# Performance work log

Measured on AMD Instinct MI355X. Metric: run time of the kernel, lower is better.

The kernel has to match this reference:

```python
import jax, jax.numpy as jnp
import numpy as np

B, T, IN, H, Z, DH, K = 512, 256, 5, 256, 128, 512, 20
OUT = 6 * K + 3


def setup_inputs() -> dict:
    key = jax.random.key(0)
    ks = jax.random.split(key, 24)
    p = lambda k, shp: jax.random.normal(k, shp, dtype=jnp.float32) * 0.05
    return {
        "s": jax.random.normal(ks[0], (B, T, IN), dtype=jnp.float32),
        "epsilon": jax.random.normal(ks[1], (Z,), dtype=jnp.float32),
        "Wih_f": p(ks[2], (4 * H, IN)), "Whh_f": p(ks[3], (4 * H, H)),
        "bih_f": p(ks[4], (4 * H,)), "bhh_f": p(ks[5], (4 * H,)),
        "Wih_b": p(ks[6], (4 * H, IN)), "Whh_b": p(ks[7], (4 * H, H)),
        "bih_b": p(ks[8], (4 * H,)), "bhh_b": p(ks[9], (4 * H,)),
        "W_sigma": p(ks[10], (Z, 2 * H)), "b_sigma": p(ks[11], (Z,)),
        "W_mu": p(ks[12], (Z, 2 * H)), "b_mu": p(ks[13], (Z,)),
        "W_h0": p(ks[14], (DH, Z)), "b_h0": p(ks[15], (DH,)),
        "Wih_d": p(ks[16], (4 * DH, IN + Z)), "Whh_d": p(ks[17], (4 * DH, DH)),
        "bih_d": p(ks[18], (4 * DH,)), "bhh_d": p(ks[19], (4 * DH,)),
        "W_dec": p(ks[20], (OUT, DH)), "b_dec": p(ks[21], (OUT,)),
    }


def _lstm_scan(x, Wih, Whh, b, reverse):
    # x: [T, B, in]; PyTorch gate order i, f, g, o
    Hh = Whh.shape[1]
    h0 = jnp.zeros((x.shape[1], Hh), x.dtype)

    def step(carry, xt):
        h, c = carry
        g = xt @ Wih.T + h @ Whh.T + b
        i, f, gg, o = jnp.split(g, 4, axis=-1)
        c = jax.nn.sigmoid(f) * c + jax.nn.sigmoid(i) * jnp.tanh(gg)
        h = jax.nn.sigmoid(o) * jnp.tanh(c)
        return (h, c), h

    _, hs = jax.lax.scan(step, (h0, h0), x, reverse=reverse)
    return hs  # [T, B, Hh]


def _mdn(y):
    # y: [..., 123] -> per-mixture (pi, mu1, mu2, sx, sy, corr) + 3 pen logits
    mix = y[..., :6 * K].reshape(y.shape[:-1] + (K, 6))
    pi = jax.nn.softmax(mix[..., 0], axis=-1)
    out_mix = jnp.stack(
        [pi, mix[..., 1], mix[..., 2], jnp.exp(mix[..., 3]),
         jnp.exp(mix[..., 4]), jnp.tanh(mix[..., 5])], axis=-1)
    pen = jax.nn.softmax(y[..., 6 * K:], axis=-1)
    return jnp.concatenate([out_mix.reshape(y.shape[:-1] + (6 * K,)), pen], axis=-1)


def reference(s, epsilon, Wih_f, Whh_f, bih_f, bhh_f, Wih_b, Whh_b, bih_b, bhh_b,
              W_sigma, b_sigma, W_mu, b_mu, W_h0, b_h0,
              Wih_d, Whh_d, bih_d, bhh_d, W_dec, b_dec):
    x = jnp.transpose(s, (1, 0, 2))  # [T, B, 5]
    hf = _lstm_scan(x, Wih_f, Whh_f, bih_f + bhh_f, False)
    hb = _lstm_scan(x, Wih_b, Whh_b, bih_b + bhh_b, True)
    h = jnp.concatenate([hf[-1], hb[-1]], axis=-1)  # output at last time step, [B, 512]
    presig = h @ W_sigma.T + b_sigma
    mu = h @ W_mu.T + b_mu
    sigma = jnp.exp(presig / 2)
    z = mu + sigma * epsilon  # [B, Z]
    h0 = jnp.tanh(z @ W_h0.T + b_h0)
    c0 = jnp.zeros((s.shape[0], DH), s.dtype)
    s0 = jnp.tile(jnp.array([0.0, 0.0, 1.0, 0.0, 0.0], s.dtype), (s.shape[0], 1))
    dec_in = jnp.concatenate([s0[None], x[:T - 1]], axis=0)  # [T, B, 5]
    bdec = bih_d + bhh_d

    def step(carry, st):
        hh, cc = carry
        xt = jnp.concatenate([st, z], axis=-1)  # [B, 133]
        g = xt @ Wih_d.T + hh @ Whh_d.T + bdec
        i, f, gg, o = jnp.split(g, 4, axis=-1)
        cc = jax.nn.sigmoid(f) * cc + jax.nn.sigmoid(i) * jnp.tanh(gg)
        hh = jax.nn.sigmoid(o) * jnp.tanh(cc)
        y = hh @ W_dec.T + b_dec
        return (hh, cc), y

    _, ys = jax.lax.scan(step, (h0, c0), dec_in)  # [T, B, 123]
    output = _mdn(jnp.transpose(ys, (1, 0, 2)))   # [B, T, 123]
    return (output, mu, presig)
```

## Files before the change

kernel.cpp:

```cpp
#include <hip/hip_runtime.h>

typedef unsigned short u16;
typedef unsigned long long u64;
typedef __attribute__((ext_vector_type(8))) short bfrag;
typedef __attribute__((ext_vector_type(4))) float f32x4;

#define MFMA __builtin_amdgcn_mfma_f32_16x16x32_bf16

#define OFF_FLAGS 0ull
#define OFF_HENC  4096ull
#define OFF_WENC  528384ull
#define OFF_WDEC  1118208ull
#define OFF_WY    3870720ull
#define OFF_WMS   4001792ull
#define OFF_WH0   4280320ull
#define OFF_HDEC  4444160ull
#define OFF_HLAT  5492736ull
#define OFF_AZ    6049792ull
#define OFF_SX    6213632ull

__device__ __forceinline__ u16 f2bf(float f) {
  union { float f; unsigned int i; } v; v.f = f;
  unsigned int r = v.i + 0x7fffu + ((v.i >> 16) & 1u);
  return (u16)(r >> 16);
}
__device__ __forceinline__ float sigm(float x) { return 1.0f / (1.0f + __expf(-x)); }
__device__ __forceinline__ float tanh_(float x) {
  float a = fabsf(x);
  float e = __expf(-2.0f * a);
  float r = (1.0f - e) / (1.0f + e);
  return x < 0.0f ? -r : r;
}

__device__ __forceinline__ u64 aload(const u64* p) {
  return __hip_atomic_load(p, __ATOMIC_RELAXED, __HIP_MEMORY_SCOPE_AGENT);
}
__device__ __forceinline__ void astore(u64* p, u64 v) {
  __hip_atomic_store(p, v, __ATOMIC_RELAXED, __HIP_MEMORY_SCOPE_AGENT);
}
__device__ __forceinline__ float afload(const float* p) {
  return __hip_atomic_load(p, __ATOMIC_RELAXED, __HIP_MEMORY_SCOPE_AGENT);
}
__device__ __forceinline__ void afstore(float* p, float v) {
  __hip_atomic_store(p, v, __ATOMIC_RELAXED, __HIP_MEMORY_SCOPE_AGENT);
}

__device__ __forceinline__ void gwait(int* base, int ep, int tid, int* sdead) {
  if (ep > 0) {
    if (tid < 32 && *sdead == 0) {
      int* fp = base + tid;
      int spin = 0;
      while (__hip_atomic_load(fp, __ATOMIC_RELAXED, __HIP_MEMORY_SCOPE_AGENT) < ep) {
        __builtin_amdgcn_s_sleep(1);
        if (++spin > (1 << 18)) { *sdead = 1; break; }
      }
    }
  }
  __syncthreads();
  asm volatile("" ::: "memory");
}
__device__ __forceinline__ void garrive(int* base, int m, int ep, int tid) {
  asm volatile("s_waitcnt vmcnt(0)" ::: "memory");
  __syncthreads();
  if (tid == 0)
    __hip_atomic_store(base + m, ep, __ATOMIC_RELAXED, __HIP_MEMORY_SCOPE_AGENT);
}

__global__ void pack_wenc(const float* __restrict__ Whh, const float* __restrict__ Wih,
                          const float* __restrict__ bi, const float* __restrict__ bh,
                          u16* __restrict__ out) {
  int idx = blockIdx.x * 256 + threadIdx.x;
  if (idx >= 294912) return;
  int m = idx / 9216, within = idx % 9216;
  int kb = within >> 10, rest = within & 1023;
  int ng = rest >> 9, l = (rest >> 3) & 63, j = rest & 7;
  int nl = ng * 16 + (l & 15);
  int u = nl >> 2, g = nl & 3;
  int row = g * 256 + m * 8 + u;
  int k = kb * 32 + (l >> 4) * 8 + j;
  float v = 0.f;
  if (k < 256) v = Whh[row * 256 + k];
  else if (k < 261) v = Wih[row * 5 + (k - 256)];
  else if (k == 261) v = bi[row] + bh[row];
  out[idx] = f2bf(v);
}

__global__ void pack_wdec(const float* __restrict__ Whh, const float* __restrict__ Wih,
                          const float* __restrict__ bi, const float* __restrict__ bh,
                          u16* __restrict__ out) {
  int idx = blockIdx.x * 256 + threadIdx.x;
  if (idx >= 1376256) return;
  int m = idx / 43008, within = idx % 43008;
  int kb = within >> 11, rest = within & 2047;
  int w = rest >> 9, l = (rest >> 3) & 63, j = rest & 7;
  int nl = w * 16 + (l & 15);
  int u = nl >> 2, g = nl & 3;
  int row = g * 512 + m * 16 + u;
  int k = kb * 32 + (l >> 4) * 8 + j;
  float v = 0.f;
  if (k < 512) v = Whh[row * 512 + k];
  else if (k < 640) v = Wih[row * 133 + 5 + (k - 512)];
  else if (k < 645) v = Wih[row * 133 + (k - 640)];
  else if (k == 645) v = bi[row] + bh[row];
  out[idx] = f2bf(v);
}

__global__ void pack_wy(const float* __restrict__ Wd, u16* __restrict__ out) {
  int idx = blockIdx.x * 256 + threadIdx.x;
  if (idx >= 65536) return;
  int m = idx >> 13, within = idx & 8191;
  int kb = within >> 9, rest = within & 511;
  int l = rest >> 3, j = rest & 7;
  int row = m * 16 + (l & 15);
  int k = kb * 32 + (l >> 4) * 8 + j;
  float v = (row < 123 && k < 512) ? Wd[row * 512 + k] : 0.f;
  out[idx] = f2bf(v);
}

__global__ void pack_wms(const float* __restrict__ Wmu, const float* __restrict__ bmu,
                         const float* __restrict__ Wsig, const float* __restrict__ bsig,
                         u16* __restrict__ out) {
  int idx = blockIdx.x * 256 + threadIdx.x;
  if (idx >= 139264) return;
  int r = idx / 544, k = idx % 544;
  float v = 0.f;
  if (r < 128) {
    if (k < 512) v = Wmu[r * 512 + k];
    else if (k == 512) v = bmu[r];
  } else {
    int r2 = r - 128;
    if (k < 512) v = Wsig[r2 * 512 + k];
    else if (k == 512) v = bsig[r2];
  }
  out[idx] = f2bf(v);
}

__global__ void pack_wh0(const float* __restrict__ Wh0, const float* __restrict__ bh0,
                         u16* __restrict__ out) {
  int idx = blockIdx.x * 256 + threadIdx.x;
  if (idx >= 81920) return;
  int r = idx / 160, k = idx % 160;
  float v = 0.f;
  if (k < 128) v = Wh0[r * 128 + k];
  else if (k == 128) v = bh0[r];
  out[idx] = f2bf(v);
}

__global__ void pack_sx(const float* __restrict__ s, u16* __restrict__ out) {
  int idx = blockIdx.x * 256 + threadIdx.x;
  if (idx >= 1048576) return;
  int j = idx & 7, b = (idx >> 3) & 511, t = idx >> 12;
  u16 v;
  if (j < 5) v = f2bf(s[((size_t)b * 256 + t) * 5 + j]);
  else v = (j == 5) ? (u16)0x3F80 : (u16)0;
  out[idx] = v;
}

__global__ __launch_bounds__(256, 1) void rnn_persist(
    int* __restrict__ flags, u16* __restrict__ henc,
    const u16* __restrict__ WENCP, const u16* __restrict__ WDECP,
    const u16* __restrict__ WYP, const u16* __restrict__ WMSP, const u16* __restrict__ WH0P,
    u16* __restrict__ hdec, u16* __restrict__ hlat, u16* __restrict__ Az,
    const u16* __restrict__ SXD,
    const float* __restrict__ s, const float* __restrict__ eps,
    const float* __restrict__ Wih_b, const float* __restrict__ bih_b,
    const float* __restrict__ bhh_b,
    const float* __restrict__ b_dec, float* __restrict__ out)
{
  __shared__ __align__(16) u16 sm[72960];
  __shared__ __align__(16) float gbuf[2112];
  __shared__ __align__(16) u16 hst[1024];
  __shared__ int sdead;

  const int tid = threadIdx.x;
  const int blk = blockIdx.x;
  const int g = blk & 7;
  const int m = blk >> 3;
  const int B0 = g * 64;
  const int w = tid >> 6, l = tid & 63;
  const int lr = l & 15, ko = (l >> 4) * 8;
  int* FA = flags + g * 128;
  int* FB = FA + 64;

  float* out_mu = out + 16121856;
  float* out_ps = out + 16187392;

  const int gcol = m * 16 + lr;
  float bd = 0.f;
  if (m < 8 && gcol < 123) bd = b_dec[gcol];

  if (tid == 0) sdead = 0;
  {
    bfrag zz = {0, 0, 0, 0, 0, 0, 0, 0};
    #pragma unroll
    for (int i = 0; i < 5; ++i) {
      int c = i * 256 + tid;
      if (c < 1184) *(bfrag*)(sm + c * 8) = zz;
    }
  }
  {
    const u16* src = WENCP + (size_t)m * 9216;
    #pragma unroll
    for (int i = 0; i < 5; ++i) {
      int c = i * 256 + tid;
      if (c < 1152) *(bfrag*)(sm + 21760 + c * 8) = *(const bfrag*)(src + c * 8);
    }
  }
  __syncthreads();

  float c_enc0 = 0.f, c_enc1 = 0.f;
  #pragma unroll 1
  for (int t = 0; t < 256; ++t) {
    #pragma unroll
    for (int X = 0; X < 2; ++X) {
      int* F = X ? FB : FA;
      gwait(F, t, tid, &sdead);
      const u64* hs = (const u64*)(henc + (size_t)((t + 1) & 1) * 131072 +
                                   (size_t)(B0 + X * 32) * 256);
      u64 hv[8];
      #pragma unroll
      for (int i = 0; i < 8; ++i) hv[i] = aload(hs + i * 256 + tid);
      #pragma unroll
      for (int i = 0; i < 8; ++i) {
        int idx = i * 256 + tid;
        *(u64*)(sm + (idx >> 6) * 296 + (idx & 63) * 4) = hv[i];
      }
      if (tid < 64) {
        int row = tid >> 1, q = tid & 1;
        *(u64*)(sm + row * 296 + 256 + q * 4) =
            *(const u64*)(SXD + ((size_t)(t * 512 + B0 + X * 32 + row)) * 8 + q * 4);
      }
      __syncthreads();
      const int mt = w >> 1, ng = w & 1;
      f32x4 acc = {0.f, 0.f, 0.f, 0.f};
      #pragma unroll
      for (int kb = 0; kb < 9; ++kb) {
        bfrag a = *(const bfrag*)(sm + (mt * 16 + lr) * 296 + kb * 32 + ko);
        bfrag bw = *(const bfrag*)(sm + 21760 + (kb * 2 + ng) * 512 + l * 8);
        acc = MFMA(a, bw, acc, 0, 0, 0);
      }
      #pragma unroll
      for (int j = 0; j < 4; ++j)
        gbuf[(mt * 16 + (l >> 4) * 4 + j) * 33 + ng * 16 + lr] = acc[j];
      __syncthreads();
      {
        int bl = tid >> 3, u = tid & 7;
        float gi = gbuf[bl * 33 + u * 4 + 0], gf = gbuf[bl * 33 + u * 4 + 1];
        float gg = gbuf[bl * 33 + u * 4 + 2], go = gbuf[bl * 33 + u * 4 + 3];
        float cprev = (X == 0) ? c_enc0 : c_enc1;
        float c = sigm(gf) * cprev + sigm(gi) * tanh_(gg);
        if (X == 0) c_enc0 = c; else c_enc1 = c;
        hst[bl * 8 + u] = f2bf(sigm(go) * tanh_(c));
      }
      __syncthreads();
      if (tid < 64) {
        int row = tid >> 1, q = tid & 1;
        u64 v = *(const u64*)(hst + row * 8 + q * 4);
        astore((u64*)(henc + (size_t)(t & 1) * 131072 +
                      (size_t)(B0 + X * 32 + row) * 256 + m * 8) + q, v);
      }
      garrive(F, m, t + 1, tid);
    }
  }

  u16* lat_hf = (u16*)gbuf;
  u16* lat_hb = (u16*)gbuf + 512;
  u16* lat_z  = (u16*)gbuf + 1024;

  gwait(FA, 256, tid, &sdead);
  gwait(FB, 256, tid, &sdead);
  {
    const u16* src = WDECP + (size_t)m * 43008;
    #pragma unroll 1
    for (int i = 0; i < 21; ++i) {
      int c = i * 256 + tid;
      *(bfrag*)(sm + 21760 + c * 8) = *(const bfrag*)(src + c * 8);
    }
  }
  if (m < 8) {
    const u16* src = WYP + (size_t)m * 8192;
    #pragma unroll
    for (int i = 0; i < 4; ++i) {
      int c = i * 256 + tid;
      *(bfrag*)(sm + 64768 + c * 8) = *(const bfrag*)(src + c * 8);
    }
  }
  #pragma unroll
  for (int r = 0; r < 2; ++r) {
    int b = B0 + m * 2 + r;
    if (tid < 64) {
      u64 v = aload((const u64*)(henc + 131072 + (size_t)b * 256) + tid);
      *(u64*)(lat_hf + r * 256 + tid * 4) = v;
    }
    {
      const float* xr = s + ((size_t)b * 256 + 255) * 5;
      float x0 = xr[0], x1 = xr[1], x2 = xr[2], x3 = xr[3], x4 = xr[4];
      int n = tid;
      float gv[4];
      #pragma unroll
      for (int gg = 0; gg < 4; ++gg) {
        int row = gg * 256 + n;
        gv[gg] = bih_b[row] + bhh_b[row] + x0 * Wih_b[row * 5] + x1 * Wih_b[row * 5 + 1] +
                 x2 * Wih_b[row * 5 + 2] + x3 * Wih_b[row * 5 + 3] + x4 * Wih_b[row * 5 + 4];
      }
      float c = sigm(gv[0]) * tanh_(gv[2]);
      lat_hb[r * 256 + n] = f2bf(sigm(gv[3]) * tanh_(c));
    }
  }
  __syncthreads();
  #pragma unroll
  for (int it = 0; it < 2; ++it) {
    int idx = it * 256 + tid;
    if (idx < 272) {
      int rr = idx / 136, u = idx % 136;
      u64 pv = 0;
      #pragma unroll
      for (int q = 0; q < 4; ++q) {
        int c = u * 4 + q;
        u16 x;
        if (c < 256) x = lat_hf[rr * 256 + c];
        else if (c < 512) x = lat_hb[rr * 256 + c - 256];
        else if (c == 512) x = 0x3F80;
        else x = 0;
        pv |= ((u64)x) << (q * 16);
      }
      astore((u64*)(hlat + (size_t)(B0 + m * 2 + rr) * 544) + u, pv);
    }
  }
  garrive(FA, m, 257, tid);

  gwait(FA, 257, tid, &sdead);
  {
    const int bH = m >> 4, cT = m & 15;
    const u64* src = (const u64*)(hlat + (size_t)(B0 + bH * 32) * 544);
    u64 sv[17];
    #pragma unroll
    for (int i = 0; i < 17; ++i) sv[i] = aload(src + i * 256 + tid);
    #pragma unroll
    for (int i = 0; i < 17; ++i) *(u64*)(sm + (i * 256 + tid) * 4) = sv[i];
    __syncthreads();
    if (w < 2) {
      f32x4 acc = {0.f, 0.f, 0.f, 0.f};
      const u16* bp = WMSP + (size_t)(cT * 16 + lr) * 544 + ko;
      #pragma unroll
      for (int kb = 0; kb < 17; ++kb) {
        bfrag a = *(const bfrag*)(sm + (w * 16 + lr) * 544 + kb * 32 + ko);
        bfrag bb = *(const bfrag*)(bp + kb * 32);
        acc = MFMA(a, bb, acc, 0, 0, 0);
      }
      int nc = cT * 16 + lr;
      #pragma unroll
      for (int j = 0; j < 4; ++j) {
        int b = B0 + bH * 32 + w * 16 + (l >> 4) * 4 + j;
        if (nc < 128) afstore(out_mu + (size_t)b * 128 + nc, acc[j]);
        else afstore(out_ps + (size_t)b * 128 + nc - 128, acc[j]);
      }
    }
  }
  garrive(FA, m, 258, tid);

  gwait(FA, 258, tid, &sdead);
  {
    int r = tid >> 7, zj = tid & 127;
    int b = B0 + m * 2 + r;
    float mu = afload(out_mu + (size_t)b * 128 + zj);
    float ps = afload(out_ps + (size_t)b * 128 + zj);
    float z = mu + __expf(0.5f * ps) * eps[zj];
    lat_z[r * 128 + zj] = f2bf(z);
  }
  __syncthreads();
  if (tid < 80) {
    int r = tid / 40, u = tid % 40;
    u64 pv = 0;
    #pragma unroll
    for (int q = 0; q < 4; ++q) {
      int c = u * 4 + q;
      u16 x;
      if (c < 128) x = lat_z[r * 128 + c];
      else if (c == 128) x = 0x3F80;
      else x = 0;
      pv |= ((u64)x) << (q * 16);
    }
    astore((u64*)(Az + (size_t)(B0 + m * 2 + r) * 160) + u, pv);
  }
  garrive(FA, m, 259, tid);

  gwait(FA, 259, tid, &sdead);
  u64 zreg0[4], zreg1[4];
  {
    int r = tid >> 3;
    #pragma unroll
    for (int i = 0; i < 4; ++i) {
      int uu = (tid & 7) * 4 + i;
      zreg0[i] = aload((const u64*)(Az + (size_t)(B0 + r) * 160) + uu);
      zreg1[i] = aload((const u64*)(Az + (size_t)(B0 + 32 + r) * 160) + uu);
    }
  }
  {
    const u64* src = (const u64*)(Az + (size_t)B0 * 160);
    u64 sv[10];
    #pragma unroll
    for (int i = 0; i < 10; ++i) sv[i] = aload(src + i * 256 + tid);
    #pragma unroll
    for (int i = 0; i < 10; ++i) *(u64*)(sm + (i * 256 + tid) * 4) = sv[i];
    __syncthreads();
    f32x4 acc = {0.f, 0.f, 0.f, 0.f};
    const u16* bp = WH0P + (size_t)(m * 16 + lr) * 160 + ko;
    #pragma unroll
    for (int kb = 0; kb < 5; ++kb) {
      bfrag a = *(const bfrag*)(sm + (w * 16 + lr) * 160 + kb * 32 + ko);
      bfrag bb = *(const bfrag*)(bp + kb * 32);
      acc = MFMA(a, bb, acc, 0, 0, 0);
    }
    #pragma unroll
    for (int j = 0; j < 4; ++j)
      hst[(w * 16 + (l >> 4) * 4 + j) * 16 + lr] = f2bf(tanh_(acc[j]));
  }
  __syncthreads();
  #pragma unroll
  for (int i = 0; i < 5; ++i) {
    int idx = i * 256 + tid;
    if (idx < 1120) {
      int row = idx / 35, c = idx % 35;
      sm[row * 680 + 645 + c] = (c == 0) ? 0x3F80 : 0;
    }
  }
  {
    int row = tid >> 2, q = tid & 3;
    u64 v = *(const u64*)(hst + row * 16 + q * 4);
    astore((u64*)(hdec + 262144 + (size_t)(B0 + row) * 512 + m * 16) + q, v);
  }
  garrive(FA, m, 260, tid);
  if (tid == 0)
    __hip_atomic_store(FB + m, 257, __ATOMIC_RELAXED, __HIP_MEMORY_SCOPE_AGENT);

  float c_dec00 = 0.f, c_dec01 = 0.f, c_dec10 = 0.f, c_dec11 = 0.f;
  #pragma unroll 1
  for (int t = 0; t < 256; ++t) {
    #pragma unroll
    for (int X = 0; X < 2; ++X) {
      int* F = X ? FB : FA;
      int base = X ? 257 : 260;
      gwait(F, base + t, tid, &sdead);
      const u64* hs = (const u64*)(hdec + (size_t)((t + 1) & 1) * 262144 +
                                   (size_t)(B0 + X * 32) * 512);
      u64 hv[16];
      #pragma unroll
      for (int i = 0; i < 16; ++i) hv[i] = aload(hs + i * 256 + tid);
      #pragma unroll
      for (int i = 0; i < 16; ++i) {
        int idx = i * 256 + tid;
        *(u64*)(sm + (idx >> 7) * 680 + (idx & 127) * 4) = hv[i];
      }
      {
        int r = tid >> 3;
        #pragma unroll
        for (int i = 0; i < 4; ++i) {
          int uu = (tid & 7) * 4 + i;
          *(u64*)(sm + r * 680 + 512 + uu * 4) = (X == 0) ? zreg0[i] : zreg1[i];
        }
      }
      if (tid < 64) {
        int row = tid >> 1, q = tid & 1;
        u64 v;
        if (t == 0) v = q ? 0x000000003F800000ULL : 0x00003F8000000000ULL;
        else v = *(const u64*)(SXD + ((size_t)((t - 1) * 512 + B0 + X * 32 + row)) * 8 + q * 4);
        *(u64*)(sm + row * 680 + 640 + q * 4) = v;
      }
      __syncthreads();
      const int mtd = w & 1, nb = (w >> 1) * 2;
      const bool doy = (m < 8) && (w < 2) && (t > 0);
      f32x4 acc0 = {0.f, 0.f, 0.f, 0.f}, acc1 = {0.f, 0.f, 0.f, 0.f}, accy = {0.f, 0.f, 0.f, 0.f};
      #pragma unroll
      for (int kb = 0; kb < 21; ++kb) {
        bfrag a  = *(const bfrag*)(sm + (mtd * 16 + lr) * 680 + kb * 32 + ko);
        bfrag b0 = *(const bfrag*)(sm + 21760 + kb * 2048 + nb * 512 + l * 8);
        bfrag b1 = *(const bfrag*)(sm + 21760 + kb * 2048 + (nb + 1) * 512 + l * 8);
        acc0 = MFMA(a, b0, acc0, 0, 0, 0);
        acc1 = MFMA(a, b1, acc1, 0, 0, 0);
        if (kb < 16 && doy) {
          bfrag by = *(const bfrag*)(sm + 64768 + kb * 512 + l * 8);
          accy = MFMA(a, by, accy, 0, 0, 0);
        }
      }
      if (doy && gcol < 123) {
        int brow = B0 + X * 32 + w * 16 + (l >> 4) * 4;
        #pragma unroll
        for (int j = 0; j < 4; ++j)
          out[((size_t)(brow + j) * 256 + (t - 1)) * 123 + gcol] = accy[j] + bd;
      }
      #pragma unroll
      for (int j = 0; j < 4; ++j) {
        int grow = mtd * 16 + (l >> 4) * 4 + j;
        gbuf[grow * 66 + nb * 16 + lr] = acc0[j];
        gbuf[grow * 66 + (nb + 1) * 16 + lr] = acc1[j];
      }
      __syncthreads();
      #pragma unroll
      for (int p = 0; p < 2; ++p) {
        int idx = p * 256 + tid;
        int bl = idx >> 4, u = idx & 15;
        float gi = gbuf[bl * 66 + u * 4 + 0], gf = gbuf[bl * 66 + u * 4 + 1];
        float gg = gbuf[bl * 66 + u * 4 + 2], go = gbuf[bl * 66 + u * 4 + 3];
        float cprev = (X == 0) ? (p == 0 ? c_dec00 : c_dec01) : (p == 0 ? c_dec10 : c_dec11);
        float c = sigm(gf) * cprev + sigm(gi) * tanh_(gg);
        if (X == 0) { if (p == 0) c_dec00 = c; else c_dec01 = c; }
        else        { if (p == 0) c_dec10 = c; else c_dec11 = c; }
        hst[bl * 16 + u] = f2bf(sigm(go) * tanh_(c));
      }
      __syncthreads();
      if (tid < 128) {
        int row = tid >> 2, q = tid & 3;
        u64 v = *(const u64*)(hst + row * 16 + q * 4);
        astore((u64*)(hdec + (size_t)(t & 1) * 262144 +
                      (size_t)(B0 + X * 32 + row) * 512 + m * 16) + q, v);
      }
      garrive(F, m, base + t + 1, tid);
    }
  }

  gwait(FA, 516, tid, &sdead);
  gwait(FB, 513, tid, &sdead);
  #pragma unroll
  for (int X = 0; X < 2; ++X) {
    const u64* hsrc = (const u64*)(hdec + 262144 + (size_t)(B0 + X * 32) * 512);
    u64 hv[16];
    #pragma unroll
    for (int i = 0; i < 16; ++i) hv[i] = aload(hsrc + i * 256 + tid);
    #pragma unroll
    for (int i = 0; i < 16; ++i) {
      int idx = i * 256 + tid;
      *(u64*)(sm + (idx >> 7) * 680 + (idx & 127) * 4) = hv[i];
    }
    __syncthreads();
    if (m < 8 && w < 2) {
      f32x4 accy = {0.f, 0.f, 0.f, 0.f};
      #pragma unroll
      for (int kb = 0; kb < 16; ++kb) {
        bfrag a = *(const bfrag*)(sm + (w * 16 + lr) * 680 + kb * 32 + ko);
        bfrag by = *(const bfrag*)(sm + 64768 + kb * 512 + l * 8);
        accy = MFMA(a, by, accy, 0, 0, 0);
      }
      if (gcol < 123) {
        int brow = B0 + X * 32 + w * 16 + (l >> 4) * 4;
        #pragma unroll
        for (int j = 0; j < 4; ++j)
          out[((size_t)(brow + j) * 256 + 255) * 123 + gcol] = accy[j] + bd;
      }
    }
    __syncthreads();
  }
}

__global__ __launch_bounds__(64) void mdn_final(float* __restrict__ out) {
  __shared__ float rows[64 * 123];
  const int tid = threadIdx.x;
  float4* g4 = (float4*)(out + (size_t)blockIdx.x * 64 * 123);
  #pragma unroll
  for (int i = 0; i < 31; ++i) {
    int c = i * 64 + tid;
    if (c < 1968) ((float4*)rows)[c] = g4[c];
  }
  __syncthreads();
  {
    float* r = rows + tid * 123;
    float m1 = -1e30f;
    #pragma unroll
    for (int k = 0; k < 20; ++k) m1 = fmaxf(m1, r[6 * k]);
    float s1 = 0.f;
    #pragma unroll
    for (int k = 0; k < 20; ++k) s1 += __expf(r[6 * k] - m1);
    float i1 = 1.f / s1;
    #pragma unroll
    for (int k = 0; k < 20; ++k) {
      r[6 * k] = __expf(r[6 * k] - m1) * i1;
      r[6 * k + 3] = __expf(r[6 * k + 3]);
      r[6 * k + 4] = __expf(r[6 * k + 4]);
      r[6 * k + 5] = tanh_(r[6 * k + 5]);
    }
    float p0 = r[120], p1 = r[121], p2 = r[122];
    float mp = fmaxf(p0, fmaxf(p1, p2));
    float e0 = __expf(p0 - mp), e1 = __expf(p1 - mp), e2 = __expf(p2 - mp);
    float ip = 1.f / (e0 + e1 + e2);
    r[120] = e0 * ip; r[121] = e1 * ip; r[122] = e2 * ip;
  }
  __syncthreads();
  #pragma unroll
  for (int i = 0; i < 31; ++i) {
    int c = i * 64 + tid;
    if (c < 1968) g4[c] = ((float4*)rows)[c];
  }
}

extern "C" void kernel_launch(void* const* d_in, const int* in_sizes, int n_in,
                              void* d_out, int out_size, void* d_ws, size_t ws_size,
                              hipStream_t stream) {
  const float* s       = (const float*)d_in[0];
  const float* eps     = (const float*)d_in[1];
  const float* Wih_f   = (const float*)d_in[2];
  const float* Whh_f   = (const float*)d_in[3];
  const float* bih_f   = (const float*)d_in[4];
  const float* bhh_f   = (const float*)d_in[5];
  const float* Wih_b   = (const float*)d_in[6];
  const float* bih_b   = (const float*)d_in[8];
  const float* bhh_b   = (const float*)d_in[9];
  const float* W_sigma = (const float*)d_in[10];
  const float* b_sigma = (const float*)d_in[11];
  const float* W_mu    = (const float*)d_in[12];
  const float* b_mu    = (const float*)d_in[13];
  const float* W_h0    = (const float*)d_in[14];
  const float* b_h0    = (const float*)d_in[15];
  const float* Wih_d   = (const float*)d_in[16];
  const float* Whh_d   = (const float*)d_in[17];
  const float* bih_d   = (const float*)d_in[18];
  const float* bhh_d   = (const float*)d_in[19];
  const float* W_dec   = (const float*)d_in[20];
  const float* b_dec   = (const float*)d_in[21];

  char* ws = (char*)d_ws;
  int* FLAGS  = (int*)(ws + OFF_FLAGS);
  u16* HENC   = (u16*)(ws + OFF_HENC);
  u16* WENCP  = (u16*)(ws + OFF_WENC);
  u16* WDECP  = (u16*)(ws + OFF_WDEC);
  u16* WYP    = (u16*)(ws + OFF_WY);
  u16* WMSP   = (u16*)(ws + OFF_WMS);
  u16* WH0P   = (u16*)(ws + OFF_WH0);
  u16* HDEC   = (u16*)(ws + OFF_HDEC);
  u16* HLAT   = (u16*)(ws + OFF_HLAT);
  u16* AZ     = (u16*)(ws + OFF_AZ);
  u16* SXD    = (u16*)(ws + OFF_SX);
  float* out  = (float*)d_out;

  hipMemsetAsync(ws, 0, 4096 + 524288, stream);

  pack_wenc<<<1152, 256, 0, stream>>>(Whh_f, Wih_f, bih_f, bhh_f, WENCP);
  pack_wdec<<<5376, 256, 0, stream>>>(Whh_d, Wih_d, bih_d, bhh_d, WDECP);
  pack_wy<<<256, 256, 0, stream>>>(W_dec, WYP);
  pack_wms<<<544, 256, 0, stream>>>(W_mu, b_mu, W_sigma, b_sigma, WMSP);
  pack_wh0<<<320, 256, 0, stream>>>(W_h0, b_h0, WH0P);
  pack_sx<<<4096, 256, 0, stream>>>(s, SXD);

  rnn_persist<<<256, 256, 0, stream>>>(FLAGS, HENC, WENCP, WDECP, WYP, WMSP, WH0P,
                                       HDEC, HLAT, AZ, SXD, s, eps,
                                       Wih_b, bih_b, bhh_b, b_dec, out);

  mdn_final<<<2048, 64, 0, stream>>>(out);

  (void)in_sizes; (void)n_in; (void)out_size; (void)ws_size;
}
```

Baseline: 2.991 ms.

## Replace per-step flag barriers with timestamp-tagged hidden-state words and prefetch

Each bf16 pair of hidden state is now stored as a 64-bit word whose high half carries the timestep tag. Consumers spin on the tags of the data itself instead of waiting on separate arrive/wait flag counters per step. The next step's hidden state and inputs are loaded right after the current step's store, so the load latency overlaps with other blocks finishing. This removes a flag round-trip per recurrent step. The cost is twice the bytes per hidden-state transfer, more registers (32 u64), and a larger memset of the workspace.

Result: no change. 2.943 ms, median of 2 (-1.6%).

```diff
diff --git a/kernel.cpp b/kernel.cpp
--- a/kernel.cpp
+++ b/kernel.cpp
@@ -1,6 +1,7 @@
 #include <hip/hip_runtime.h>
 
 typedef unsigned short u16;
+typedef unsigned int u32;
 typedef unsigned long long u64;
 typedef __attribute__((ext_vector_type(8))) short bfrag;
 typedef __attribute__((ext_vector_type(4))) float f32x4;
@@ -8,16 +9,17 @@
 #define MFMA __builtin_amdgcn_mfma_f32_16x16x32_bf16
 
 #define OFF_FLAGS 0ull
-#define OFF_HENC  4096ull
-#define OFF_WENC  528384ull
-#define OFF_WDEC  1118208ull
-#define OFF_WY    3870720ull
-#define OFF_WMS   4001792ull
-#define OFF_WH0   4280320ull
-#define OFF_HDEC  4444160ull
-#define OFF_HLAT  5492736ull
-#define OFF_AZ    6049792ull
-#define OFF_SX    6213632ull
+#define OFF_HENCW 4096ull
+#define OFF_HDECW 1052672ull
+#define MEMSET_BYTES 3149824ull
+#define OFF_WENC  3149824ull
+#define OFF_WDEC  3739648ull
+#define OFF_WY    6492160ull
+#define OFF_WMS   6623232ull
+#define OFF_WH0   6901760ull
+#define OFF_HLAT  7065600ull
+#define OFF_AZ    7622656ull
+#define OFF_SX    7786496ull
 
 __device__ __forceinline__ u16 f2bf(float f) {
   union { float f; unsigned int i; } v; v.f = f;
@@ -157,11 +159,10 @@
 }
 
 __global__ __launch_bounds__(256, 1) void rnn_persist(
-    int* __restrict__ flags, u16* __restrict__ henc,
+    int* __restrict__ flags, u64* __restrict__ hencW, u64* __restrict__ hdecW,
     const u16* __restrict__ WENCP, const u16* __restrict__ WDECP,
     const u16* __restrict__ WYP, const u16* __restrict__ WMSP, const u16* __restrict__ WH0P,
-    u16* __restrict__ hdec, u16* __restrict__ hlat, u16* __restrict__ Az,
-    const u16* __restrict__ SXD,
+    u16* __restrict__ hlat, u16* __restrict__ Az, const u16* __restrict__ SXD,
     const float* __restrict__ s, const float* __restrict__ eps,
     const float* __restrict__ Wih_b, const float* __restrict__ bih_b,
     const float* __restrict__ bhh_b,
@@ -179,8 +180,8 @@
   const int B0 = g * 64;
   const int w = tid >> 6, l = tid & 63;
   const int lr = l & 15, ko = (l >> 4) * 8;
-  int* FA = flags + g * 128;
-  int* FB = FA + 64;
+  int* FG = flags + g * 64;
+  const u32* hst32 = (const u32*)hst;
 
   float* out_mu = out + 16121856;
   float* out_ps = out + 16187392;
@@ -208,67 +209,83 @@
   }
   __syncthreads();
 
+  u64 hv[32];
+  u64 sxv = 0;
+
+  {
+    const u64* base = hencW + 65536 + (size_t)B0 * 128;
+    #pragma unroll
+    for (int i = 0; i < 16; ++i) hv[i] = aload(base + i * 256 + tid);
+    if (tid < 64)
+      sxv = *(const u64*)(SXD + (size_t)(B0 + (tid >> 1)) * 8 + (tid & 1) * 4);
+  }
   float c_enc0 = 0.f, c_enc1 = 0.f;
   #pragma unroll 1
-  for (int t = 0; t < 256; ++t) {
-    #pragma unroll
-    for (int X = 0; X < 2; ++X) {
-      int* F = X ? FB : FA;
-      gwait(F, t, tid, &sdead);
-      const u64* hs = (const u64*)(henc + (size_t)((t + 1) & 1) * 131072 +
-                                   (size_t)(B0 + X * 32) * 256);
-      u64 hv[8];
-      #pragma unroll
-      for (int i = 0; i < 8; ++i) hv[i] = aload(hs + i * 256 + tid);
-      #pragma unroll
-      for (int i = 0; i < 8; ++i) {
-        int idx = i * 256 + tid;
-        *(u64*)(sm + (idx >> 6) * 296 + (idx & 63) * 4) = hv[i];
-      }
-      if (tid < 64) {
-        int row = tid >> 1, q = tid & 1;
-        *(u64*)(sm + row * 296 + 256 + q * 4) =
-            *(const u64*)(SXD + ((size_t)(t * 512 + B0 + X * 32 + row)) * 8 + q * 4);
-      }
-      __syncthreads();
-      const int mt = w >> 1, ng = w & 1;
-      f32x4 acc = {0.f, 0.f, 0.f, 0.f};
-      #pragma unroll
-      for (int kb = 0; kb < 9; ++kb) {
-        bfrag a = *(const bfrag*)(sm + (mt * 16 + lr) * 296 + kb * 32 + ko);
-        bfrag bw = *(const bfrag*)(sm + 21760 + (kb * 2 + ng) * 512 + l * 8);
-        acc = MFMA(a, bw, acc, 0, 0, 0);
-      }
-      #pragma unroll
-      for (int j = 0; j < 4; ++j)
-        gbuf[(mt * 16 + (l >> 4) * 4 + j) * 33 + ng * 16 + lr] = acc[j];
-      __syncthreads();
-      {
-        int bl = tid >> 3, u = tid & 7;
-        float gi = gbuf[bl * 33 + u * 4 + 0], gf = gbuf[bl * 33 + u * 4 + 1];
-        float gg = gbuf[bl * 33 + u * 4 + 2], go = gbuf[bl * 33 + u * 4 + 3];
-        float cprev = (X == 0) ? c_enc0 : c_enc1;
-        float c = sigm(gf) * cprev + sigm(gi) * tanh_(gg);
-        if (X == 0) c_enc0 = c; else c_enc1 = c;
-        hst[bl * 8 + u] = f2bf(sigm(go) * tanh_(c));
-      }
-      __syncthreads();
-      if (tid < 64) {
-        int row = tid >> 1, q = tid & 1;
-        u64 v = *(const u64*)(hst + row * 8 + q * 4);
-        astore((u64*)(henc + (size_t)(t & 1) * 131072 +
-                      (size_t)(B0 + X * 32 + row) * 256 + m * 8) + q, v);
-      }
-      garrive(F, m, t + 1, tid);
+  for (int e = 0; e < 512; ++e) {
+    const int X = e & 1, t = e >> 1;
+    {
+      const u64* base = hencW + (size_t)((t + 1) & 1) * 65536 + (size_t)(B0 + X * 32) * 128;
+      int tries = 0;
+      while (true) {
+        bool ok = true;
+        #pragma unroll
+        for (int i = 0; i < 16; ++i) ok &= ((u32)(hv[i] >> 32) == (u32)t);
+        if (__all(ok)) break;
+        if (++tries > (1 << 14)) break;
+        __builtin_amdgcn_s_sleep(1);
+        #pragma unroll
+        for (int i = 0; i < 16; ++i) hv[i] = aload(base + i * 256 + tid);
+      }
+    }
+    #pragma unroll
+    for (int i = 0; i < 16; ++i) {
+      int idx = i * 256 + tid;
+      *(u32*)((char*)sm + (idx >> 7) * 592 + (idx & 127) * 4) = (u32)hv[i];
+    }
+    if (tid < 64) *(u64*)(sm + (tid >> 1) * 296 + 256 + (tid & 1) * 4) = sxv;
+    __syncthreads();
+    const int mt = w >> 1, ng = w & 1;
+    f32x4 acc = {0.f, 0.f, 0.f, 0.f};
+    #pragma unroll
+    for (int kb = 0; kb < 9; ++kb) {
+      bfrag a = *(const bfrag*)(sm + (mt * 16 + lr) * 296 + kb * 32 + ko);
+      bfrag bw = *(const bfrag*)(sm + 21760 + (kb * 2 + ng) * 512 + l * 8);
+      acc = MFMA(a, bw, acc, 0, 0, 0);
+    }
+    #pragma unroll
+    for (int j = 0; j < 4; ++j)
+      gbuf[(mt * 16 + (l >> 4) * 4 + j) * 33 + ng * 16 + lr] = acc[j];
+    __syncthreads();
+    {
+      int bl = tid >> 3, u = tid & 7;
+      float gi = gbuf[bl * 33 + u * 4 + 0], gf = gbuf[bl * 33 + u * 4 + 1];
+      float gg = gbuf[bl * 33 + u * 4 + 2], go = gbuf[bl * 33 + u * 4 + 3];
+      float cprev = (X == 0) ? c_enc0 : c_enc1;
+      float c = sigm(gf) * cprev + sigm(gi) * tanh_(gg);
+      if (X == 0) c_enc0 = c; else c_enc1 = c;
+      hst[bl * 8 + u] = f2bf(sigm(go) * tanh_(c));
+    }
+    __syncthreads();
+    if (tid < 128) {
+      int row = tid >> 2, j = tid & 3;
+      u64 wv = (u64)hst32[row * 4 + j] | ((u64)(u32)(t + 1) << 32);
+      astore(hencW + (size_t)(t & 1) * 65536 + (size_t)(B0 + X * 32 + row) * 128 + 4 * m + j, wv);
+    }
+    if (e < 511) {
+      int Xn = (e + 1) & 1, tn = (e + 1) >> 1;
+      const u64* base = hencW + (size_t)((tn + 1) & 1) * 65536 + (size_t)(B0 + Xn * 32) * 128;
+      #pragma unroll
+      for (int i = 0; i < 16; ++i) hv[i] = aload(base + i * 256 + tid);
+      if (tid < 64)
+        sxv = *(const u64*)(SXD + (size_t)(tn * 512 + B0 + Xn * 32 + (tid >> 1)) * 8 + (tid & 1) * 4);
     }
   }
 
   u16* lat_hf = (u16*)gbuf;
   u16* lat_hb = (u16*)gbuf + 512;
   u16* lat_z  = (u16*)gbuf + 1024;
-
-  gwait(FA, 256, tid, &sdead);
-  gwait(FB, 256, tid, &sdead);
+  __syncthreads();
+
   {
     const u16* src = WDECP + (size_t)m * 43008;
     #pragma unroll 1
@@ -285,27 +302,33 @@
       *(bfrag*)(sm + 64768 + c * 8) = *(const bfrag*)(src + c * 8);
     }
   }
+  {
+    int r = tid >> 7, wc = tid & 127;
+    const u64* p = hencW + 65536 + (size_t)(B0 + m * 2 + r) * 128 + wc;
+    u64 v = aload(p);
+    int tries = 0;
+    while (!__all((u32)(v >> 32) == 256u)) {
+      if (++tries > (1 << 14)) break;
+      __builtin_amdgcn_s_sleep(1);
+      v = aload(p);
+    }
+    ((u32*)lat_hf)[r * 128 + wc] = (u32)v;
+  }
   #pragma unroll
   for (int r = 0; r < 2; ++r) {
     int b = B0 + m * 2 + r;
-    if (tid < 64) {
-      u64 v = aload((const u64*)(henc + 131072 + (size_t)b * 256) + tid);
-      *(u64*)(lat_hf + r * 256 + tid * 4) = v;
-    }
-    {
-      const float* xr = s + ((size_t)b * 256 + 255) * 5;
-      float x0 = xr[0], x1 = xr[1], x2 = xr[2], x3 = xr[3], x4 = xr[4];
-      int n = tid;
-      float gv[4];
-      #pragma unroll
-      for (int gg = 0; gg < 4; ++gg) {
-        int row = gg * 256 + n;
-        gv[gg] = bih_b[row] + bhh_b[row] + x0 * Wih_b[row * 5] + x1 * Wih_b[row * 5 + 1] +
-                 x2 * Wih_b[row * 5 + 2] + x3 * Wih_b[row * 5 + 3] + x4 * Wih_b[row * 5 + 4];
-      }
-      float c = sigm(gv[0]) * tanh_(gv[2]);
-      lat_hb[r * 256 + n] = f2bf(sigm(gv[3]) * tanh_(c));
-    }
+    const float* xr = s + ((size_t)b * 256 + 255) * 5;
+    float x0 = xr[0], x1 = xr[1], x2 = xr[2], x3 = xr[3], x4 = xr[4];
+    int n = tid;
+    float gv[4];
+    #pragma unroll
+    for (int gg = 0; gg < 4; ++gg) {
+      int row = gg * 256 + n;
+      gv[gg] = bih_b[row] + bhh_b[row] + x0 * Wih_b[row * 5] + x1 * Wih_b[row * 5 + 1] +
+               x2 * Wih_b[row * 5 + 2] + x3 * Wih_b[row * 5 + 3] + x4 * Wih_b[row * 5 + 4];
+    }
+    float c = sigm(gv[0]) * tanh_(gv[2]);
+    lat_hb[r * 256 + n] = f2bf(sigm(gv[3]) * tanh_(c));
   }
   __syncthreads();
   #pragma unroll
@@ -327,9 +350,8 @@
       astore((u64*)(hlat + (size_t)(B0 + m * 2 + rr) * 544) + u, pv);
     }
   }
-  garrive(FA, m, 257, tid);
-
-  gwait(FA, 257, tid, &sdead);
+  garrive(FG, m, 1, tid);
+  gwait(FG, 1, tid, &sdead);
   {
     const int bH = m >> 4, cT = m & 15;
     const u64* src = (const u64*)(hlat + (size_t)(B0 + bH * 32) * 544);
@@ -357,9 +379,8 @@
       }
     }
   }
-  garrive(FA, m, 258, tid);
-
-  gwait(FA, 258, tid, &sdead);
+  garrive(FG, m, 2, tid);
+  gwait(FG, 2, tid, &sdead);
   {
     int r = tid >> 7, zj = tid & 127;
     int b = B0 + m * 2 + r;
@@ -383,9 +404,8 @@
     }
     astore((u64*)(Az + (size_t)(B0 + m * 2 + r) * 160) + u, pv);
   }
-  garrive(FA, m, 259, tid);
-
-  gwait(FA, 259, tid, &sdead);
+  garrive(FG, m, 3, tid);
+  gwait(FG, 3, tid, &sdead);
   u64 zreg0[4], zreg1[4];
   {
     int r = tid >> 3;
@@ -418,119 +438,147 @@
   }
   __syncthreads();
   #pragma unroll
-  for (int i = 0; i < 5; ++i) {
+  for (int i = 0; i < 2; ++i) {
     int idx = i * 256 + tid;
-    if (idx < 1120) {
-      int row = idx / 35, c = idx % 35;
-      sm[row * 680 + 645 + c] = (c == 0) ? 0x3F80 : 0;
-    }
-  }
-  {
-    int row = tid >> 2, q = tid & 3;
-    u64 v = *(const u64*)(hst + row * 16 + q * 4);
-    astore((u64*)(hdec + 262144 + (size_t)(B0 + row) * 512 + m * 16) + q, v);
-  }
-  garrive(FA, m, 260, tid);
-  if (tid == 0)
-    __hip_atomic_store(FB + m, 257, __ATOMIC_RELAXED, __HIP_MEMORY_SCOPE_AGENT);
-
-  float c_dec00 = 0.f, c_dec01 = 0.f, c_dec10 = 0.f, c_dec11 = 0.f;
+    int row = idx >> 3, j = idx & 7;
+    u64 wv = (u64)hst32[row * 8 + j] | (1ull << 32);
+    astore(hdecW + 131072 + (size_t)(B0 + row) * 256 + 8 * m + j, wv);
+  }
+  #pragma unroll
+  for (int i = 0; i < 4; ++i) {
+    int idx = i * 256 + tid;
+    if (idx < 1024) {
+      int row = idx >> 5, c = idx & 31;
+      sm[row * 680 + 648 + c] = 0;
+    }
+  }
+  garrive(FG, m, 4, tid);
+  gwait(FG, 4, tid, &sdead);
+
+  {
+    const u64* base = hdecW + 131072 + (size_t)B0 * 256;
+    #pragma unroll
+    for (int i = 0; i < 32; ++i) hv[i] = aload(base + i * 256 + tid);
+    if (tid < 64)
+      sxv = *(const u64*)(SXD + (size_t)(B0 + (tid >> 1)) * 8 + (tid & 1) * 4);
+  }
+  float c00 = 0.f, c01 = 0.f, c10 = 0.f, c11 = 0.f;
   #pragma unroll 1
-  for (int t = 0; t < 256; ++t) {
-    #pragma unroll
-    for (int X = 0; X < 2; ++X) {
-      int* F = X ? FB : FA;
-      int base = X ? 257 : 260;
-      gwait(F, base + t, tid, &sdead);
-      const u64* hs = (const u64*)(hdec + (size_t)((t + 1) & 1) * 262144 +
-                                   (size_t)(B0 + X * 32) * 512);
-      u64 hv[16];
-      #pragma unroll
-      for (int i = 0; i < 16; ++i) hv[i] = aload(hs + i * 256 + tid);
-      #pragma unroll
-      for (int i = 0; i < 16; ++i) {
-        int idx = i * 256 + tid;
-        *(u64*)(sm + (idx >> 7) * 680 + (idx & 127) * 4) = hv[i];
-      }
-      {
-        int r = tid >> 3;
+  for (int e = 0; e < 512; ++e) {
+    const int X = e & 1, t = e >> 1;
+    {
+      const u64* base = hdecW + (size_t)((t + 1) & 1) * 131072 + (size_t)(B0 + X * 32) * 256;
+      int tries = 0;
+      while (true) {
+        bool ok = true;
         #pragma unroll
-        for (int i = 0; i < 4; ++i) {
-          int uu = (tid & 7) * 4 + i;
-          *(u64*)(sm + r * 680 + 512 + uu * 4) = (X == 0) ? zreg0[i] : zreg1[i];
-        }
-      }
+        for (int i = 0; i < 32; ++i) ok &= ((u32)(hv[i] >> 32) == (u32)(t + 1));
+        if (__all(ok)) break;
+        if (++tries > (1 << 14)) break;
+        __builtin_amdgcn_s_sleep(1);
+        #pragma unroll
+        for (int i = 0; i < 32; ++i) hv[i] = aload(base + i * 256 + tid);
+      }
+    }
+    #pragma unroll
+    for (int i = 0; i < 32; ++i) {
+      int idx = i * 256 + tid;
+      *(u32*)((char*)sm + (idx >> 8) * 1360 + (idx & 255) * 4) = (u32)hv[i];
+    }
+    {
+      int r = tid >> 3;
+      #pragma unroll
+      for (int i = 0; i < 4; ++i) {
+        int uu = (tid & 7) * 4 + i;
+        *(u64*)(sm + r * 680 + 512 + uu * 4) = (X == 0) ? zreg0[i] : zreg1[i];
+      }
+    }
+    if (tid < 64) {
+      u64 v = sxv;
+      if (t == 0) v = (tid & 1) ? 0x000000003F800000ULL : 0x00003F8000000000ULL;
+      *(u64*)(sm + (tid >> 1) * 680 + 640 + (tid & 1) * 4) = v;
+    }
+    __syncthreads();
+    const int mtd = w & 1, nb = (w >> 1) * 2;
+    const bool doy = (m < 8) && (w < 2) && (t > 0);
+    f32x4 acc0 = {0.f, 0.f, 0.f, 0.f}, acc1 = {0.f, 0.f, 0.f, 0.f}, accy = {0.f, 0.f, 0.f, 0.f};
+    #pragma unroll
+    for (int kb = 0; kb < 21; ++kb) {
+      bfrag a  = *(const bfrag*)(sm + (mtd * 16 + lr) * 680 + kb * 32 + ko);
+      bfrag b0 = *(const bfrag*)(sm + 21760 + kb * 2048 + nb * 512 + l * 8);
+      bfrag b1 = *(const bfrag*)(sm + 21760 + kb * 2048 + (nb + 1) * 512 + l * 8);
+      acc0 = MFMA(a, b0, acc0, 0, 0, 0);
+      acc1 = MFMA(a, b1, acc1, 0, 0, 0);
+      if (kb < 16 && doy) {
+        bfrag by = *(const bfrag*)(sm + 64768 + kb * 512 + l * 8);
+        accy = MFMA(a, by, accy, 0, 0, 0);
+      }
+    }
+    if (doy && gcol < 123) {
+      int brow = B0 + X * 32 + w * 16 + (l >> 4) * 4;
+      #pragma unroll
+      for (int j = 0; j < 4; ++j)
+        out[((size_t)(brow + j) * 256 + (t - 1)) * 123 + gcol] = accy[j] + bd;
+    }
+    #pragma unroll
+    for (int j = 0; j < 4; ++j) {
+      int grow = mtd * 16 + (l >> 4) * 4 + j;
+      gbuf[grow * 66 + nb * 16 + lr] = acc0[j];
+      gbuf[grow * 66 + (nb + 1) * 16 + lr] = acc1[j];
+    }
+    __syncthreads();
+    #pragma unroll
+    for (int p = 0; p < 2; ++p) {
+      int idx = p * 256 + tid;
+      int bl = idx >> 4, u = idx & 15;
+      float gi = gbuf[bl * 66 + u * 4 + 0], gf = gbuf[bl * 66 + u * 4 + 1];
+      float gg = gbuf[bl * 66 + u * 4 + 2], go = gbuf[bl * 66 + u * 4 + 3];
+      float cprev = (X == 0) ? (p == 0 ? c00 : c01) : (p == 0 ? c10 : c11);
+      float c = sigm(gf) * cprev + sigm(gi) * tanh_(gg);
+      if (X == 0) { if (p == 0) c00 = c; else c01 = c; }
+      else        { if (p == 0) c10 = c; else c11 = c; }
+      hst[bl * 16 + u] = f2bf(sigm(go) * tanh_(c));
+    }
+    __syncthreads();
+    {
+      int row = tid >> 3, j = tid & 7;
+      u64 wv = (u64)hst32[row * 8 + j] | ((u64)(u32)(t + 2) << 32);
+      astore(hdecW + (size_t)(t & 1) * 131072 + (size_t)(B0 + X * 32 + row) * 256 + 8 * m + j, wv);
+    }
+    if (e < 511) {
+      int Xn = (e + 1) & 1, tn = (e + 1) >> 1;
+      const u64* base = hdecW + (size_t)((tn + 1) & 1) * 131072 + (size_t)(B0 + Xn * 32) * 256;
+      #pragma unroll
+      for (int i = 0; i < 32; ++i) hv[i] = aload(base + i * 256 + tid);
       if (tid < 64) {
-        int row = tid >> 1, q = tid & 1;
-        u64 v;
-        if (t == 0) v = q ? 0x000000003F800000ULL : 0x00003F8000000000ULL;
-        else v = *(const u64*)(SXD + ((size_t)((t - 1) * 512 + B0 + X * 32 + row)) * 8 + q * 4);
-        *(u64*)(sm + row * 680 + 640 + q * 4) = v;
-      }
-      __syncthreads();
-      const int mtd = w & 1, nb = (w >> 1) * 2;
-      const bool doy = (m < 8) && (w < 2) && (t > 0);
-      f32x4 acc0 = {0.f, 0.f, 0.f, 0.f}, acc1 = {0.f, 0.f, 0.f, 0.f}, accy = {0.f, 0.f, 0.f, 0.f};
-      #pragma unroll
-      for (int kb = 0; kb < 21; ++kb) {
-        bfrag a  = *(const bfrag*)(sm + (mtd * 16 + lr) * 680 + kb * 32 + ko);
-        bfrag b0 = *(const bfrag*)(sm + 21760 + kb * 2048 + nb * 512 + l * 8);
-        bfrag b1 = *(const bfrag*)(sm + 21760 + kb * 2048 + (nb + 1) * 512 + l * 8);
-        acc0 = MFMA(a, b0, acc0, 0, 0, 0);
-        acc1 = MFMA(a, b1, acc1, 0, 0, 0);
-        if (kb < 16 && doy) {
-          bfrag by = *(const bfrag*)(sm + 64768 + kb * 512 + l * 8);
-          accy = MFMA(a, by, accy, 0, 0, 0);
-        }
-      }
-      if (doy && gcol < 123) {
-        int brow = B0 + X * 32 + w * 16 + (l >> 4) * 4;
+        int tp = (tn > 0) ? (tn - 1) : 0;
+        sxv = *(const u64*)(SXD + (size_t)(tp * 512 + B0 + Xn * 32 + (tid >> 1)) * 8 + (tid & 1) * 4);
+      }
+    }
+  }
+
+  #pragma unroll 1
+  for (int hh = 0; hh < 2; ++hh) {
+    const u64* base = hdecW + 131072 + (size_t)(B0 + hh * 32) * 256;
+    #pragma unroll
+    for (int i = 0; i < 32; ++i) hv[i] = aload(base + i * 256 + tid);
+    {
+      int tries = 0;
+      while (true) {
+        bool ok = true;
         #pragma unroll
-        for (int j = 0; j < 4; ++j)
-          out[((size_t)(brow + j) * 256 + (t - 1)) * 123 + gcol] = accy[j] + bd;
-      }
-      #pragma unroll
-      for (int j = 0; j < 4; ++j) {
-        int grow = mtd * 16 + (l >> 4) * 4 + j;
-        gbuf[grow * 66 + nb * 16 + lr] = acc0[j];
-        gbuf[grow * 66 + (nb + 1) * 16 + lr] = acc1[j];
-      }
-      __syncthreads();
-      #pragma unroll
-      for (int p = 0; p < 2; ++p) {
-        int idx = p * 256 + tid;
-        int bl = idx >> 4, u = idx & 15;
-        float gi = gbuf[bl * 66 + u * 4 + 0], gf = gbuf[bl * 66 + u * 4 + 1];
-        float gg = gbuf[bl * 66 + u * 4 + 2], go = gbuf[bl * 66 + u * 4 + 3];
-        float cprev = (X == 0) ? (p == 0 ? c_dec00 : c_dec01) : (p == 0 ? c_dec10 : c_dec11);
-        float c = sigm(gf) * cprev + sigm(gi) * tanh_(gg);
-        if (X == 0) { if (p == 0) c_dec00 = c; else c_dec01 = c; }
-        else        { if (p == 0) c_dec10 = c; else c_dec11 = c; }
-        hst[bl * 16 + u] = f2bf(sigm(go) * tanh_(c));
-      }
-      __syncthreads();
-      if (tid < 128) {
-        int row = tid >> 2, q = tid & 3;
-        u64 v = *(const u64*)(hst + row * 16 + q * 4);
-        astore((u64*)(hdec + (size_t)(t & 1) * 262144 +
-                      (size_t)(B0 + X * 32 + row) * 512 + m * 16) + q, v);
-      }
-      garrive(F, m, base + t + 1, tid);
-    }
-  }
-
-  gwait(FA, 516, tid, &sdead);
-  gwait(FB, 513, tid, &sdead);
-  #pragma unroll
-  for (int X = 0; X < 2; ++X) {
-    const u64* hsrc = (const u64*)(hdec + 262144 + (size_t)(B0 + X * 32) * 512);
-    u64 hv[16];
-    #pragma unroll
-    for (int i = 0; i < 16; ++i) hv[i] = aload(hsrc + i * 256 + tid);
-    #pragma unroll
-    for (int i = 0; i < 16; ++i) {
+        for (int i = 0; i < 32; ++i) ok &= ((u32)(hv[i] >> 32) == 257u);
+        if (__all(ok)) break;
+        if (++tries > (1 << 14)) break;
+        __builtin_amdgcn_s_sleep(1);
+        #pragma unroll
+        for (int i = 0; i < 32; ++i) hv[i] = aload(base + i * 256 + tid);
+      }
+    }
+    #pragma unroll
+    for (int i = 0; i < 32; ++i) {
       int idx = i * 256 + tid;
-      *(u64*)(sm + (idx >> 7) * 680 + (idx & 127) * 4) = hv[i];
+      *(u32*)((char*)sm + (idx >> 8) * 1360 + (idx & 255) * 4) = (u32)hv[i];
     }
     __syncthreads();
     if (m < 8 && w < 2) {
@@ -542,7 +590,7 @@
         accy = MFMA(a, by, accy, 0, 0, 0);
       }
       if (gcol < 123) {
-        int brow = B0 + X * 32 + w * 16 + (l >> 4) * 4;
+        int brow = B0 + hh * 32 + w * 16 + (l >> 4) * 4;
         #pragma unroll
         for (int j = 0; j < 4; ++j)
           out[((size_t)(brow + j) * 256 + 255) * 123 + gcol] = accy[j] + bd;
@@ -619,19 +667,19 @@
 
   char* ws = (char*)d_ws;
   int* FLAGS  = (int*)(ws + OFF_FLAGS);
-  u16* HENC   = (u16*)(ws + OFF_HENC);
+  u64* HENCW  = (u64*)(ws + OFF_HENCW);
+  u64* HDECW  = (u64*)(ws + OFF_HDECW);
   u16* WENCP  = (u16*)(ws + OFF_WENC);
   u16* WDECP  = (u16*)(ws + OFF_WDEC);
   u16* WYP    = (u16*)(ws + OFF_WY);
   u16* WMSP   = (u16*)(ws + OFF_WMS);
   u16* WH0P   = (u16*)(ws + OFF_WH0);
-  u16* HDEC   = (u16*)(ws + OFF_HDEC);
   u16* HLAT   = (u16*)(ws + OFF_HLAT);
   u16* AZ     = (u16*)(ws + OFF_AZ);
   u16* SXD    = (u16*)(ws + OFF_SX);
   float* out  = (float*)d_out;
 
-  hipMemsetAsync(ws, 0, 4096 + 524288, stream);
+  hipMemsetAsync(ws, 0, (size_t)MEMSET_BYTES, stream);
 
   pack_wenc<<<1152, 256, 0, stream>>>(Whh_f, Wih_f, bih_f, bhh_f, WENCP);
   pack_wdec<<<5376, 256, 0, stream>>>(Whh_d, Wih_d, bih_d, bhh_d, WDECP);
@@ -640,8 +688,8 @@
   pack_wh0<<<320, 256, 0, stream>>>(W_h0, b_h0, WH0P);
   pack_sx<<<4096, 256, 0, stream>>>(s, SXD);
 
-  rnn_persist<<<256, 256, 0, stream>>>(FLAGS, HENC, WENCP, WDECP, WYP, WMSP, WH0P,
-                                       HDEC, HLAT, AZ, SXD, s, eps,
+  rnn_persist<<<256, 256, 0, stream>>>(FLAGS, HENCW, HDECW, WENCP, WDECP, WYP, WMSP, WH0P,
+                                       HLAT, AZ, SXD, s, eps,
                                        Wih_b, bih_b, bhh_b, b_dec, out);
 
   mdn_final<<<2048, 64, 0, stream>>>(out);
```
